# Kernel tuning notes

Measured on AMD Instinct MI355X. Metric: run time of the kernel, lower is better.

Reference implementation:

```python
import jax, jax.numpy as jnp
import numpy as np

R, E, N, B = 64, 100000, 1000000, 4

def setup_inputs() -> dict:
    key = jax.random.key(0)
    k1, k2, k3 = jax.random.split(key, 3)
    p = jax.random.normal(k1, (R,), dtype=jnp.float32)
    edges = jax.random.randint(k2, (R, E, 2), 0, N, dtype=jnp.int64)
    x = jax.random.normal(k3, (B, N), dtype=jnp.float32)
    return {"p": p, "edges": edges, "x": x}

def reference(p, edges, x):
    # _A = sum_r p[r] * (A_r + A_r^T), with A_r[u,v] += 1 per edge (duplicates sum,
    # matching scipy csr_matrix construction). y = x @ _A, i.e.
    # y[b, j] = sum over edges (u,v) of relation r: p[r]*x[b,u] into j=v and p[r]*x[b,v] into j=u.
    num_entities = x.shape[1]
    e = edges.shape[1]
    src = edges[..., 0].reshape(-1)            # [R*E]
    dst = edges[..., 1].reshape(-1)            # [R*E]
    w = jnp.repeat(p, e)                       # [R*E] per-edge relation weight
    # include inverse edges
    srcs = jnp.concatenate([src, dst])         # [2RE]
    dsts = jnp.concatenate([dst, src])         # [2RE]
    ww = jnp.concatenate([w, w])               # [2RE]
    vals = x[:, srcs].T * ww[:, None]          # [2RE, B] gathered & weighted messages
    y = jax.ops.segment_sum(vals, dsts, num_segments=num_entities).T  # [B, N]
    return y
```

## Files before the change

kernel.cpp:

```cpp
#include <hip/hip_runtime.h>
#include <hip/hip_fp16.h>


constexpr int  R_   = 64;
constexpr long E_   = 100000;
constexpr int  N_   = 1000000;
constexpr long RE_  = (long)R_ * E_;
constexpr long M2_  = 2 * RE_;
constexpr int  BSH  = 11;
constexpr int  BUCKET = 1 << BSH;
constexpr int  NB   = (N_ + BUCKET - 1) >> BSH;
constexpr int  NBP  = 512;
constexpr int  EPB  = 4096;
constexpr int  HB   = (int)((RE_ + EPB - 1) / EPB);
constexpr int  RPB  = 2 * EPB;
constexpr int  CH   = 8192;


__global__ __launch_bounds__(256) void k_hist(const int2* __restrict__ edges,
                                              int* __restrict__ g_bcnt) {
    __shared__ int lc[NB];
    for (int i = threadIdx.x; i < NB; i += 256) lc[i] = 0;
    __syncthreads();
    long k0 = (long)blockIdx.x * EPB;
    int lim = (int)min((long)EPB, RE_ - k0);
    for (int i = threadIdx.x; i < lim; i += 256) {
        int2 e = edges[k0 + i];
        atomicAdd(&lc[e.y >> BSH], 1);
        atomicAdd(&lc[e.x >> BSH], 1);
    }
    __syncthreads();
    for (int c = threadIdx.x; c < NB; c += 256)
        g_bcnt[(size_t)c * HB + blockIdx.x] = lc[c];
}

__global__ __launch_bounds__(256) void k_cellscan(const int* __restrict__ g_bcnt,
                                                  int* __restrict__ g_bbase,
                                                  int* __restrict__ ctot) {
    __shared__ int sA[256], sB[256];
    const int c = blockIdx.x, t = threadIdx.x;
    int run = 0;
    for (int chunk = 0; chunk < HB; chunk += 256) {
        int b = chunk + t;
        int v = (b < HB) ? g_bcnt[(size_t)c * HB + b] : 0;
        sA[t] = v;
        __syncthreads();
        int* A = sA; int* B = sB;
        for (int off = 1; off < 256; off <<= 1) {
            int xv = A[t];
            if (t >= off) xv += A[t - off];
            B[t] = xv;
            __syncthreads();
            int* tmp = A; A = B; B = tmp;
        }
        int incl = A[t];
        if (b < HB) g_bbase[(size_t)c * HB + b] = run + incl - v;
        run += A[255];
        __syncthreads();
    }
    if (t == 0) ctot[c] = run;
}

__global__ __launch_bounds__(512) void k_scan(const int* __restrict__ ctot,
                                              int* __restrict__ cbase) {
    __shared__ int sA[NBP], sB[NBP];
    int t = threadIdx.x;
    sA[t] = (t < NB) ? ctot[t] : 0;
    __syncthreads();
    int* A = sA; int* B = sB;
    for (int off = 1; off < NBP; off <<= 1) {
        int xv = A[t];
        if (t >= off) xv += A[t - off];
        B[t] = xv;
        __syncthreads();
        int* tmp = A; A = B; B = tmp;
    }
    if (t < NB) cbase[t] = t ? A[t - 1] : 0;
    if (t == 0) cbase[NB] = A[NB - 1];
}


__global__ __launch_bounds__(1024) void k_srcbin(const int2* __restrict__ edges,
                                                 const int* __restrict__ g_bcnt,
                                                 const int* __restrict__ g_bbase,
                                                 const int* __restrict__ cbase,
                                                 unsigned short* __restrict__ g_sl,
                                                 unsigned* __restrict__ g_dr) {
    __shared__ unsigned l_src[RPB];
    __shared__ unsigned l_dr[RPB];
    __shared__ int sA[NBP], sB[NBP];
    __shared__ int excl[NB], cur[NB], gbase[NB];
    const int t = threadIdx.x, blk = blockIdx.x;
    if (t < NBP) {
        int v = 0;
        if (t < NB) {
            v = g_bcnt[(size_t)t * HB + blk];
            gbase[t] = cbase[t] + g_bbase[(size_t)t * HB + blk];
        }
        sA[t] = v;
    }
    __syncthreads();
    int* A = sA; int* B = sB;
    for (int off = 1; off < NBP; off <<= 1) {
        if (t < NBP) { int v = A[t]; if (t >= off) v += A[t - off]; B[t] = v; }
        __syncthreads();
        int* tmp = A; A = B; B = tmp;
    }
    if (t < NB) { int e = t ? A[t - 1] : 0; excl[t] = e; cur[t] = e; }
    __syncthreads();

    long k0 = (long)blk * EPB;
    int lim = (int)min((long)EPB, RE_ - k0);
    for (int i = t; i < lim; i += 1024) {
        int2 e = edges[k0 + i];
        unsigned r = (unsigned)(k0 + i) / (unsigned)E_;
        int c1 = e.x >> BSH;
        int s1 = atomicAdd(&cur[c1], 1);
        l_src[s1] = (unsigned)e.x;
        l_dr[s1]  = (unsigned)e.y | (r << 20);
        int c2 = e.y >> BSH;
        int s2 = atomicAdd(&cur[c2], 1);
        l_src[s2] = (unsigned)e.y;
        l_dr[s2]  = (unsigned)e.x | (r << 20);
    }
    __syncthreads();
    int total = 2 * lim;
    for (int s = t; s < total; s += 1024) {
        unsigned src = l_src[s];
        int c = (int)(src >> BSH);
        int pos = gbase[c] + (s - excl[c]);
        g_sl[pos] = (unsigned short)(src & (BUCKET - 1));
        __builtin_nontemporal_store(l_dr[s], g_dr + pos);
    }
}


__global__ __launch_bounds__(256) void k_pairhist(const unsigned* __restrict__ g_dr,
                                                  const int* __restrict__ cbase,
                                                  int* __restrict__ pairT) {
    __shared__ int lc[NB];
    const int s = blockIdx.x, t = threadIdx.x;
    for (int i = t; i < NB; i += 256) lc[i] = 0;
    __syncthreads();
    const int lo = cbase[s], hi = cbase[s + 1];
    for (int i = lo + t; i < hi; i += 256) {
        int d = (int)((g_dr[i] & 0xFFFFFu) >> BSH);
        atomicAdd(&lc[d], 1);
    }
    __syncthreads();
    for (int d = t; d < NB; d += 256) pairT[(size_t)d * NB + s] = lc[d];
}

__global__ __launch_bounds__(512) void k_pairscan(const int* __restrict__ cbase,
                                                  int* __restrict__ pairT) {
    __shared__ int sA[NBP], sB[NBP];
    const int d = blockIdx.x, t = threadIdx.x;
    sA[t] = (t < NB) ? pairT[(size_t)d * NB + t] : 0;
    __syncthreads();
    int* A = sA; int* B = sB;
    for (int off = 1; off < NBP; off <<= 1) {
        int v = A[t]; if (t >= off) v += A[t - off]; B[t] = v;
        __syncthreads();
        int* tmp = A; A = B; B = tmp;
    }
    if (t < NB) pairT[(size_t)d * NB + t] = cbase[d] + (t ? A[t - 1] : 0);
}


__global__ __launch_bounds__(1024) void k_msgbuild(const unsigned* __restrict__ g_dr,
                                                   const unsigned short* __restrict__ g_sl,
                                                   const int* __restrict__ cbase,
                                                   const int* __restrict__ pairT,
                                                   const float* __restrict__ p,
                                                   const float* __restrict__ x,
                                                   unsigned short* __restrict__ g_dst2,
                                                   uint2* __restrict__ g_pay2) {
    __shared__ unsigned short l_cell[CH];
    __shared__ unsigned short l_dl[CH];
    __shared__ uint2 l_pay[CH];
    __shared__ uint2 xl[BUCKET];
    __shared__ int sA[NBP], sB[NBP];
    __shared__ int excl[NB], cur[NB], runbase[NB];
    __shared__ float pl[R_];
    const int t = threadIdx.x, s = blockIdx.x;
    if (t < R_) pl[t] = p[t];
    for (int j = t; j < BUCKET; j += 1024) {
        int g = (s << BSH) + j;
        float v0 = 0.f, v1 = 0.f, v2 = 0.f, v3 = 0.f;
        if (g < N_) {
            v0 = x[g]; v1 = x[(long)N_ + g]; v2 = x[2L * N_ + g]; v3 = x[3L * N_ + g];
        }
        __half2 a = __floats2half2_rn(v0, v1);
        __half2 b = __floats2half2_rn(v2, v3);
        xl[j] = make_uint2(__builtin_bit_cast(unsigned, a),
                           __builtin_bit_cast(unsigned, b));
    }
    for (int d = t; d < NB; d += 1024) runbase[d] = pairT[(size_t)d * NB + s];
    __syncthreads();

    const int lo = cbase[s], hi = cbase[s + 1];
    for (int i0 = lo; i0 < hi; i0 += CH) {
        const int cn = min(CH, hi - i0);
        for (int i = t; i < NBP; i += 1024) sA[i] = 0;
        __syncthreads();
        unsigned short mc[8], mdl[8];
        uint2 mp[8];
        #pragma unroll
        for (int j = 0; j < 8; ++j) {
            int k = t + j * 1024;
            mc[j] = 0xFFFF;
            if (k < cn) {
                unsigned dr = g_dr[i0 + k];
                unsigned short sl = g_sl[i0 + k];
                unsigned dst = dr & 0xFFFFFu;
                int c = (int)(dst >> BSH);
                float w = pl[dr >> 20];
                uint2 xv = xl[sl];
                __half2 h0 = __builtin_bit_cast(__half2, xv.x);
                __half2 h1 = __builtin_bit_cast(__half2, xv.y);
                mp[j] = make_uint2(
                    __builtin_bit_cast(unsigned, __floats2half2_rn(w * __low2float(h0), w * __high2float(h0))),
                    __builtin_bit_cast(unsigned, __floats2half2_rn(w * __low2float(h1), w * __high2float(h1))));
                mdl[j] = (unsigned short)(dst & (BUCKET - 1));
                mc[j]  = (unsigned short)c;
                atomicAdd(&sA[c], 1);
            }
        }
        __syncthreads();
        {
            int* A = sA; int* B = sB;
            for (int off = 1; off < NBP; off <<= 1) {
                if (t < NBP) { int v = A[t]; if (t >= off) v += A[t - off]; B[t] = v; }
                __syncthreads();
                int* tmp = A; A = B; B = tmp;
            }
            if (t < NB) { int e = t ? A[t - 1] : 0; excl[t] = e; cur[t] = e; }
        }
        __syncthreads();
        #pragma unroll
        for (int j = 0; j < 8; ++j) {
            if (mc[j] != 0xFFFF) {
                int pos = atomicAdd(&cur[mc[j]], 1);
                l_cell[pos] = mc[j];
                l_dl[pos]   = mdl[j];
                l_pay[pos]  = mp[j];
            }
        }
        __syncthreads();
        for (int s2 = t; s2 < cn; s2 += 1024) {
            int c = l_cell[s2];
            int gpos = runbase[c] + (s2 - excl[c]);
            g_dst2[gpos] = l_dl[s2];
            unsigned long long pk = ((unsigned long long)l_pay[s2].y << 32) | l_pay[s2].x;
            __builtin_nontemporal_store(pk, (unsigned long long*)g_pay2 + gpos);
        }
        __syncthreads();
        for (int d = t; d < NB; d += 1024) runbase[d] += cur[d] - excl[d];
        __syncthreads();
    }
}


__global__ __launch_bounds__(1024) void k_accum(const unsigned short* __restrict__ g_dst,
                                                const uint2* __restrict__ g_pay,
                                                const int* __restrict__ cbase,
                                                float* __restrict__ y) {
    __shared__ unsigned long long accA[BUCKET];
    __shared__ unsigned long long accB[BUCKET];
    const int t = threadIdx.x, b = blockIdx.x;
    for (int i = t; i < BUCKET; i += 1024) { accA[i] = 0ull; accB[i] = 0ull; }
    __syncthreads();
    const int lo = cbase[b], hi = cbase[b + 1];
    for (int i = lo + t; i < hi; i += 1024) {
        int dl = (int)g_dst[i];
        uint2 pay = g_pay[i];
        __half2 h01 = __builtin_bit_cast(__half2, pay.x);
        __half2 h23 = __builtin_bit_cast(__half2, pay.y);
        float f0 = fminf(fmaxf(__low2float(h01),  -31.f), 31.f);
        float f1 = fminf(fmaxf(__high2float(h01), -31.f), 31.f);
        float f2 = fminf(fmaxf(__low2float(h23),  -31.f), 31.f);
        float f3 = fminf(fmaxf(__high2float(h23), -31.f), 31.f);
        unsigned e0 = (unsigned)(__float2int_rn(f0 * 65536.f) + (1 << 21));
        unsigned e1 = (unsigned)(__float2int_rn(f1 * 65536.f) + (1 << 21));
        unsigned e2 = (unsigned)(__float2int_rn(f2 * 65536.f) + (1 << 21));
        unsigned e3 = (unsigned)(__float2int_rn(f3 * 65536.f) + (1 << 21));
        unsigned long long va = (unsigned long long)e0
                              | ((unsigned long long)e1 << 28)
                              | (1ull << 56);
        unsigned long long vb = (unsigned long long)e2
                              | ((unsigned long long)e3 << 28);
        atomicAdd(&accA[dl], va);
        atomicAdd(&accB[dl], vb);
    }
    __syncthreads();
    const int base_e = b << BSH;
    for (int j = t; j < BUCKET; j += 1024) {
        int i = base_e + j;
        if (i < N_) {
            unsigned long long a = accA[j], bb = accB[j];
            long deg  = (long)(a >> 56);
            long bias = deg << 21;
            long c0 = (long)(a & 0xFFFFFFFull) - bias;
            long c1 = (long)((a >> 28) & 0xFFFFFFFull) - bias;
            long c2 = (long)(bb & 0xFFFFFFFull) - bias;
            long c3 = (long)((bb >> 28) & 0xFFFFFFFull) - bias;
            const float sc = 1.f / 65536.f;
            y[i]            = (float)c0 * sc;
            y[(long)N_ + i] = (float)c1 * sc;
            y[2L * N_ + i]  = (float)c2 * sc;
            y[3L * N_ + i]  = (float)c3 * sc;
        }
    }
}


__global__ __launch_bounds__(256) void k_transpose_h(const float* __restrict__ x,
                                                     uint2* __restrict__ xTh) {
    int i = blockIdx.x * 256 + threadIdx.x;
    if (i < N_) {
        __half2 a = __floats2half2_rn(x[i],           x[(long)N_ + i]);
        __half2 b = __floats2half2_rn(x[2L * N_ + i], x[3L * N_ + i]);
        xTh[i] = make_uint2(__builtin_bit_cast(unsigned, a),
                            __builtin_bit_cast(unsigned, b));
    }
}

__global__ __launch_bounds__(1024) void k_bin_g(const int2* __restrict__ edges,
                                                const float* __restrict__ p,
                                                const uint2* __restrict__ xTh,
                                                const int* __restrict__ g_bcnt,
                                                const int* __restrict__ g_bbase,
                                                const int* __restrict__ cbase,
                                                unsigned short* __restrict__ g_dst,
                                                uint2* __restrict__ g_pay) {
    __shared__ int   ldst[RPB];
    __shared__ uint2 lpay[RPB];
    __shared__ int sA[NBP], sB[NBP];
    __shared__ int excl[NB], cur[NB], gbase[NB];
    __shared__ float pl[R_];
    const int t = threadIdx.x, blk = blockIdx.x;
    if (t < NBP) {
        int v = 0;
        if (t < NB) {
            v = g_bcnt[(size_t)t * HB + blk];
            gbase[t] = cbase[t] + g_bbase[(size_t)t * HB + blk];
        }
        sA[t] = v;
    }
    if (t < R_) pl[t] = p[t];
    __syncthreads();
    int* A = sA; int* B = sB;
    for (int off = 1; off < NBP; off <<= 1) {
        if (t < NBP) { int xv = A[t]; if (t >= off) xv += A[t - off]; B[t] = xv; }
        __syncthreads();
        int* tmp = A; A = B; B = tmp;
    }
    if (t < NB) { int e = t ? A[t - 1] : 0; excl[t] = e; cur[t] = e; }
    __syncthreads();
    long k0 = (long)blk * EPB;
    int lim = (int)min((long)EPB, RE_ - k0);
    for (int i = t; i < lim; i += 1024) {
        int2 e = edges[k0 + i];
        float w = pl[(unsigned)(k0 + i) / (unsigned)E_];
        uint2 xu = xTh[e.x];
        uint2 xv = xTh[e.y];
        __half2 a0 = __builtin_bit_cast(__half2, xu.x);
        __half2 a1 = __builtin_bit_cast(__half2, xu.y);
        uint2 pv = make_uint2(
            __builtin_bit_cast(unsigned, __floats2half2_rn(w * __low2float(a0), w * __high2float(a0))),
            __builtin_bit_cast(unsigned, __floats2half2_rn(w * __low2float(a1), w * __high2float(a1))));
        __half2 b0 = __builtin_bit_cast(__half2, xv.x);
        __half2 b1 = __builtin_bit_cast(__half2, xv.y);
        uint2 pu = make_uint2(
            __builtin_bit_cast(unsigned, __floats2half2_rn(w * __low2float(b0), w * __high2float(b0))),
            __builtin_bit_cast(unsigned, __floats2half2_rn(w * __low2float(b1), w * __high2float(b1))));
        int cy = e.y >> BSH;
        int s1 = atomicAdd(&cur[cy], 1);
        ldst[s1] = e.y;
        lpay[s1] = pv;
        int cx = e.x >> BSH;
        int s2 = atomicAdd(&cur[cx], 1);
        ldst[s2] = e.x;
        lpay[s2] = pu;
    }
    __syncthreads();
    int total = 2 * lim;
    for (int s = t; s < total; s += 1024) {
        int dst = ldst[s];
        int c = dst >> BSH;
        int pos = gbase[c] + (s - excl[c]);
        g_dst[pos] = (unsigned short)(dst & (BUCKET - 1));
        g_pay[pos] = lpay[s];
    }
}


__global__ __launch_bounds__(256) void k_scatter_direct(const int2* __restrict__ edges,
                                                        const float* __restrict__ p,
                                                        const float* __restrict__ x,
                                                        float* __restrict__ y) {
    const long stride = (long)gridDim.x * blockDim.x;
    for (long k = (long)blockIdx.x * blockDim.x + threadIdx.x; k < RE_; k += stride) {
        int2 e = edges[k];
        float w = p[(int)(k / E_)];
        #pragma unroll
        for (int b = 0; b < 4; ++b) {
            float xu = x[(long)b * N_ + e.x];
            float xv = x[(long)b * N_ + e.y];
            atomicAdd(&y[(long)b * N_ + e.y], w * xu);
            atomicAdd(&y[(long)b * N_ + e.x], w * xv);
        }
    }
}

extern "C" void kernel_launch(void* const* d_in, const int* in_sizes, int n_in,
                              void* d_out, int out_size, void* d_ws, size_t ws_size,
                              hipStream_t stream) {
    const float* p     = (const float*)d_in[0];
    const int*   edges = (const int*)d_in[1];
    const float* x     = (const float*)d_in[2];
    float*       y     = (float*)d_out;

    const size_t pay_bytes   = (size_t)M2_ * 8;
    const size_t dr_bytes    = (size_t)M2_ * 4;
    const size_t sl_bytes    = (size_t)M2_ * 2;
    const size_t dst2_bytes  = (size_t)M2_ * 2;
    const size_t bcnt_bytes  = (size_t)NB * HB * 4;
    const size_t pair_bytes  = (size_t)NB * NB * 4;
    const size_t ctot_bytes  = (size_t)NB * 4;
    const size_t cbase_bytes = (size_t)(NB + 1) * 4;
    const size_t xTh_bytes   = (size_t)N_ * 8;

    const size_t need_new = pay_bytes + dr_bytes + sl_bytes + dst2_bytes
                          + 2 * bcnt_bytes + pair_bytes + ctot_bytes + cbase_bytes;
    const size_t need_r8  = xTh_bytes + pay_bytes + dst2_bytes
                          + 2 * bcnt_bytes + ctot_bytes + cbase_bytes;

    if (ws_size >= need_new) {
        char* ws = (char*)d_ws;
        uint2* g_pay2 = (uint2*)ws;                  ws += pay_bytes;
        unsigned* g_dr = (unsigned*)ws;              ws += dr_bytes;
        int* g_bcnt  = (int*)ws;                     ws += bcnt_bytes;
        int* g_bbase = (int*)ws;                     ws += bcnt_bytes;
        int* pairT   = (int*)ws;                     ws += pair_bytes;
        int* ctot    = (int*)ws;                     ws += ctot_bytes;
        int* cbase   = (int*)ws;                     ws += cbase_bytes;
        unsigned short* g_sl   = (unsigned short*)ws; ws += sl_bytes;
        unsigned short* g_dst2 = (unsigned short*)ws;

        k_hist<<<HB, 256, 0, stream>>>((const int2*)edges, g_bcnt);
        k_cellscan<<<NB, 256, 0, stream>>>(g_bcnt, g_bbase, ctot);
        k_scan<<<1, 512, 0, stream>>>(ctot, cbase);
        k_srcbin<<<HB, 1024, 0, stream>>>((const int2*)edges, g_bcnt, g_bbase,
                                          cbase, g_sl, g_dr);
        k_pairhist<<<NB, 256, 0, stream>>>((const unsigned*)g_dr, cbase, pairT);
        k_pairscan<<<NB, 512, 0, stream>>>(cbase, pairT);
        k_msgbuild<<<NB, 1024, 0, stream>>>((const unsigned*)g_dr,
                                            (const unsigned short*)g_sl,
                                            cbase, pairT, p, x, g_dst2, g_pay2);
        k_accum<<<NB, 1024, 0, stream>>>((const unsigned short*)g_dst2,
                                         (const uint2*)g_pay2, cbase, y);
    } else if (ws_size >= need_r8) {
        char* ws = (char*)d_ws;
        uint2* xTh   = (uint2*)ws;                   ws += xTh_bytes;
        uint2* g_pay = (uint2*)ws;                   ws += pay_bytes;
        int* g_bcnt  = (int*)ws;                     ws += bcnt_bytes;
        int* g_bbase = (int*)ws;                     ws += bcnt_bytes;
        int* ctot    = (int*)ws;                     ws += ctot_bytes;
        int* cbase   = (int*)ws;                     ws += cbase_bytes;
        unsigned short* g_dst = (unsigned short*)ws;

        k_transpose_h<<<(N_ + 255) / 256, 256, 0, stream>>>(x, xTh);
        k_hist<<<HB, 256, 0, stream>>>((const int2*)edges, g_bcnt);
        k_cellscan<<<NB, 256, 0, stream>>>(g_bcnt, g_bbase, ctot);
        k_scan<<<1, 512, 0, stream>>>(ctot, cbase);
        k_bin_g<<<HB, 1024, 0, stream>>>((const int2*)edges, p, (const uint2*)xTh,
                                         g_bcnt, g_bbase, cbase, g_dst, g_pay);
        k_accum<<<NB, 1024, 0, stream>>>((const unsigned short*)g_dst,
                                         (const uint2*)g_pay, cbase, y);
    } else {
        hipMemsetAsync(y, 0, (size_t)out_size * sizeof(float), stream);
        k_scatter_direct<<<8192, 256, 0, stream>>>((const int2*)edges, p, x, y);
    }
}
```

Baseline: 273.1 us.

## Stage only 16-bit indices in LDS for binning and re-read global data on scatter

In k_srcbin and k_msgbuild the per-entry LDS staging of full records (src, dst|rel, cell, dst-local, half payload) is replaced by a 16-bit index permutation. During the scatter pass the edge or dr/sl data is re-read from global memory and the payload is computed at that point. The smaller LDS footprint permits doubling the msgbuild chunk size CH to 16384. The unused xTh fallback path is removed. This trades LDS capacity and bandwidth for extra, partly uncoalesced, global re-reads that are likely to hit in cache.

```diff
diff --git a/kernel.cpp b/kernel.cpp
--- a/kernel.cpp
+++ b/kernel.cpp
@@ -14,7 +14,7 @@
 constexpr int  EPB  = 4096;
 constexpr int  HB   = (int)((RE_ + EPB - 1) / EPB);
 constexpr int  RPB  = 2 * EPB;
-constexpr int  CH   = 8192;
+constexpr int  CH   = 16384;
 
 
 __global__ __launch_bounds__(256) void k_hist(const int2* __restrict__ edges,
@@ -86,8 +86,7 @@
                                                  const int* __restrict__ cbase,
                                                  unsigned short* __restrict__ g_sl,
                                                  unsigned* __restrict__ g_dr) {
-    __shared__ unsigned l_src[RPB];
-    __shared__ unsigned l_dr[RPB];
+    __shared__ unsigned short l_idx[RPB];
     __shared__ int sA[NBP], sB[NBP];
     __shared__ int excl[NB], cur[NB], gbase[NB];
     const int t = threadIdx.x, blk = blockIdx.x;
@@ -109,28 +108,33 @@
     if (t < NB) { int e = t ? A[t - 1] : 0; excl[t] = e; cur[t] = e; }
     __syncthreads();
 
-    long k0 = (long)blk * EPB;
-    int lim = (int)min((long)EPB, RE_ - k0);
-    for (int i = t; i < lim; i += 1024) {
+    const long k0 = (long)blk * EPB;
+    const int lim = (int)min((long)EPB, RE_ - k0);
+    #pragma unroll
+    for (int j = 0; j < EPB / 1024; ++j) {
+        int i = t + j * 1024;
+        if (i < lim) {
+            int2 e = edges[k0 + i];
+            int p1 = atomicAdd(&cur[e.x >> BSH], 1);
+            l_idx[p1] = (unsigned short)(2 * i);
+            int p2 = atomicAdd(&cur[e.y >> BSH], 1);
+            l_idx[p2] = (unsigned short)(2 * i + 1);
+        }
+    }
+    __syncthreads();
+    const int total = 2 * lim;
+    #pragma unroll 4
+    for (int s = t; s < total; s += 1024) {
+        int idx = l_idx[s];
+        int i = idx >> 1;
         int2 e = edges[k0 + i];
         unsigned r = (unsigned)(k0 + i) / (unsigned)E_;
-        int c1 = e.x >> BSH;
-        int s1 = atomicAdd(&cur[c1], 1);
-        l_src[s1] = (unsigned)e.x;
-        l_dr[s1]  = (unsigned)e.y | (r << 20);
-        int c2 = e.y >> BSH;
-        int s2 = atomicAdd(&cur[c2], 1);
-        l_src[s2] = (unsigned)e.y;
-        l_dr[s2]  = (unsigned)e.x | (r << 20);
-    }
-    __syncthreads();
-    int total = 2 * lim;
-    for (int s = t; s < total; s += 1024) {
-        unsigned src = l_src[s];
-        int c = (int)(src >> BSH);
+        int src, dst;
+        if (idx & 1) { src = e.y; dst = e.x; } else { src = e.x; dst = e.y; }
+        int c = src >> BSH;
         int pos = gbase[c] + (s - excl[c]);
         g_sl[pos] = (unsigned short)(src & (BUCKET - 1));
-        __builtin_nontemporal_store(l_dr[s], g_dr + pos);
+        __builtin_nontemporal_store((unsigned)dst | (r << 20), g_dr + pos);
     }
 }
 
@@ -174,10 +178,8 @@
                                                    const float* __restrict__ p,
                                                    const float* __restrict__ x,
                                                    unsigned short* __restrict__ g_dst2,
-                                                   uint2* __restrict__ g_pay2) {
-    __shared__ unsigned short l_cell[CH];
-    __shared__ unsigned short l_dl[CH];
-    __shared__ uint2 l_pay[CH];
+                                                   unsigned long long* __restrict__ g_pay2) {
+    __shared__ unsigned short l_idx[CH];
     __shared__ uint2 xl[BUCKET];
     __shared__ int sA[NBP], sB[NBP];
     __shared__ int excl[NB], cur[NB], runbase[NB];
@@ -201,28 +203,16 @@
     const int lo = cbase[s], hi = cbase[s + 1];
     for (int i0 = lo; i0 < hi; i0 += CH) {
         const int cn = min(CH, hi - i0);
-        for (int i = t; i < NBP; i += 1024) sA[i] = 0;
-        __syncthreads();
-        unsigned short mc[8], mdl[8];
-        uint2 mp[8];
+        if (t < NBP) sA[t] = 0;
+        __syncthreads();
+        unsigned short mc[CH / 1024];
         #pragma unroll
-        for (int j = 0; j < 8; ++j) {
+        for (int j = 0; j < CH / 1024; ++j) {
             int k = t + j * 1024;
             mc[j] = 0xFFFF;
             if (k < cn) {
-                unsigned dr = g_dr[i0 + k];
-                unsigned short sl = g_sl[i0 + k];
-                unsigned dst = dr & 0xFFFFFu;
-                int c = (int)(dst >> BSH);
-                float w = pl[dr >> 20];
-                uint2 xv = xl[sl];
-                __half2 h0 = __builtin_bit_cast(__half2, xv.x);
-                __half2 h1 = __builtin_bit_cast(__half2, xv.y);
-                mp[j] = make_uint2(
-                    __builtin_bit_cast(unsigned, __floats2half2_rn(w * __low2float(h0), w * __high2float(h0))),
-                    __builtin_bit_cast(unsigned, __floats2half2_rn(w * __low2float(h1), w * __high2float(h1))));
-                mdl[j] = (unsigned short)(dst & (BUCKET - 1));
-                mc[j]  = (unsigned short)c;
+                int c = (int)((g_dr[i0 + k] & 0xFFFFFu) >> BSH);
+                mc[j] = (unsigned short)c;
                 atomicAdd(&sA[c], 1);
             }
         }
@@ -238,21 +228,32 @@
         }
         __syncthreads();
         #pragma unroll
-        for (int j = 0; j < 8; ++j) {
+        for (int j = 0; j < CH / 1024; ++j) {
             if (mc[j] != 0xFFFF) {
                 int pos = atomicAdd(&cur[mc[j]], 1);
-                l_cell[pos] = mc[j];
-                l_dl[pos]   = mdl[j];
-                l_pay[pos]  = mp[j];
+                l_idx[pos] = (unsigned short)(t + j * 1024);
             }
         }
         __syncthreads();
+        #pragma unroll 4
         for (int s2 = t; s2 < cn; s2 += 1024) {
-            int c = l_cell[s2];
+            int idx = l_idx[s2];
+            unsigned dr = g_dr[i0 + idx];
+            unsigned short sl = g_sl[i0 + idx];
+            unsigned dst = dr & 0xFFFFFu;
+            int c = (int)(dst >> BSH);
+            float w = pl[dr >> 20];
+            uint2 xv = xl[sl];
+            __half2 h0 = __builtin_bit_cast(__half2, xv.x);
+            __half2 h1 = __builtin_bit_cast(__half2, xv.y);
+            unsigned plo = __builtin_bit_cast(unsigned,
+                __floats2half2_rn(w * __low2float(h0), w * __high2float(h0)));
+            unsigned phi = __builtin_bit_cast(unsigned,
+                __floats2half2_rn(w * __low2float(h1), w * __high2float(h1)));
             int gpos = runbase[c] + (s2 - excl[c]);
-            g_dst2[gpos] = l_dl[s2];
-            unsigned long long pk = ((unsigned long long)l_pay[s2].y << 32) | l_pay[s2].x;
-            __builtin_nontemporal_store(pk, (unsigned long long*)g_pay2 + gpos);
+            g_dst2[gpos] = (unsigned short)(dst & (BUCKET - 1));
+            __builtin_nontemporal_store(((unsigned long long)phi << 32) | plo,
+                                        g_pay2 + gpos);
         }
         __syncthreads();
         for (int d = t; d < NB; d += 1024) runbase[d] += cur[d] - excl[d];
@@ -314,87 +315,6 @@
 }
 
 
-__global__ __launch_bounds__(256) void k_transpose_h(const float* __restrict__ x,
-                                                     uint2* __restrict__ xTh) {
-    int i = blockIdx.x * 256 + threadIdx.x;
-    if (i < N_) {
-        __half2 a = __floats2half2_rn(x[i],           x[(long)N_ + i]);
-        __half2 b = __floats2half2_rn(x[2L * N_ + i], x[3L * N_ + i]);
-        xTh[i] = make_uint2(__builtin_bit_cast(unsigned, a),
-                            __builtin_bit_cast(unsigned, b));
-    }
-}
-
-__global__ __launch_bounds__(1024) void k_bin_g(const int2* __restrict__ edges,
-                                                const float* __restrict__ p,
-                                                const uint2* __restrict__ xTh,
-                                                const int* __restrict__ g_bcnt,
-                                                const int* __restrict__ g_bbase,
-                                                const int* __restrict__ cbase,
-                                                unsigned short* __restrict__ g_dst,
-                                                uint2* __restrict__ g_pay) {
-    __shared__ int   ldst[RPB];
-    __shared__ uint2 lpay[RPB];
-    __shared__ int sA[NBP], sB[NBP];
-    __shared__ int excl[NB], cur[NB], gbase[NB];
-    __shared__ float pl[R_];
-    const int t = threadIdx.x, blk = blockIdx.x;
-    if (t < NBP) {
-        int v = 0;
-        if (t < NB) {
-            v = g_bcnt[(size_t)t * HB + blk];
-            gbase[t] = cbase[t] + g_bbase[(size_t)t * HB + blk];
-        }
-        sA[t] = v;
-    }
-    if (t < R_) pl[t] = p[t];
-    __syncthreads();
-    int* A = sA; int* B = sB;
-    for (int off = 1; off < NBP; off <<= 1) {
-        if (t < NBP) { int xv = A[t]; if (t >= off) xv += A[t - off]; B[t] = xv; }
-        __syncthreads();
-        int* tmp = A; A = B; B = tmp;
-    }
-    if (t < NB) { int e = t ? A[t - 1] : 0; excl[t] = e; cur[t] = e; }
-    __syncthreads();
-    long k0 = (long)blk * EPB;
-    int lim = (int)min((long)EPB, RE_ - k0);
-    for (int i = t; i < lim; i += 1024) {
-        int2 e = edges[k0 + i];
-        float w = pl[(unsigned)(k0 + i) / (unsigned)E_];
-        uint2 xu = xTh[e.x];
-        uint2 xv = xTh[e.y];
-        __half2 a0 = __builtin_bit_cast(__half2, xu.x);
-        __half2 a1 = __builtin_bit_cast(__half2, xu.y);
-        uint2 pv = make_uint2(
-            __builtin_bit_cast(unsigned, __floats2half2_rn(w * __low2float(a0), w * __high2float(a0))),
-            __builtin_bit_cast(unsigned, __floats2half2_rn(w * __low2float(a1), w * __high2float(a1))));
-        __half2 b0 = __builtin_bit_cast(__half2, xv.x);
-        __half2 b1 = __builtin_bit_cast(__half2, xv.y);
-        uint2 pu = make_uint2(
-            __builtin_bit_cast(unsigned, __floats2half2_rn(w * __low2float(b0), w * __high2float(b0))),
-            __builtin_bit_cast(unsigned, __floats2half2_rn(w * __low2float(b1), w * __high2float(b1))));
-        int cy = e.y >> BSH;
-        int s1 = atomicAdd(&cur[cy], 1);
-        ldst[s1] = e.y;
-        lpay[s1] = pv;
-        int cx = e.x >> BSH;
-        int s2 = atomicAdd(&cur[cx], 1);
-        ldst[s2] = e.x;
-        lpay[s2] = pu;
-    }
-    __syncthreads();
-    int total = 2 * lim;
-    for (int s = t; s < total; s += 1024) {
-        int dst = ldst[s];
-        int c = dst >> BSH;
-        int pos = gbase[c] + (s - excl[c]);
-        g_dst[pos] = (unsigned short)(dst & (BUCKET - 1));
-        g_pay[pos] = lpay[s];
-    }
-}
-
-
 __global__ __launch_bounds__(256) void k_scatter_direct(const int2* __restrict__ edges,
                                                         const float* __restrict__ p,
                                                         const float* __restrict__ x,
@@ -429,16 +349,13 @@
     const size_t pair_bytes  = (size_t)NB * NB * 4;
     const size_t ctot_bytes  = (size_t)NB * 4;
     const size_t cbase_bytes = (size_t)(NB + 1) * 4;
-    const size_t xTh_bytes   = (size_t)N_ * 8;
-
-    const size_t need_new = pay_bytes + dr_bytes + sl_bytes + dst2_bytes
-                          + 2 * bcnt_bytes + pair_bytes + ctot_bytes + cbase_bytes;
-    const size_t need_r8  = xTh_bytes + pay_bytes + dst2_bytes
-                          + 2 * bcnt_bytes + ctot_bytes + cbase_bytes;
-
-    if (ws_size >= need_new) {
+
+    const size_t need = pay_bytes + dr_bytes + sl_bytes + dst2_bytes
+                      + 2 * bcnt_bytes + pair_bytes + ctot_bytes + cbase_bytes;
+
+    if (ws_size >= need) {
         char* ws = (char*)d_ws;
-        uint2* g_pay2 = (uint2*)ws;                  ws += pay_bytes;
+        unsigned long long* g_pay2 = (unsigned long long*)ws;  ws += pay_bytes;
         unsigned* g_dr = (unsigned*)ws;              ws += dr_bytes;
         int* g_bcnt  = (int*)ws;                     ws += bcnt_bytes;
         int* g_bbase = (int*)ws;                     ws += bcnt_bytes;
@@ -460,24 +377,6 @@
                                             cbase, pairT, p, x, g_dst2, g_pay2);
         k_accum<<<NB, 1024, 0, stream>>>((const unsigned short*)g_dst2,
                                          (const uint2*)g_pay2, cbase, y);
-    } else if (ws_size >= need_r8) {
-        char* ws = (char*)d_ws;
-        uint2* xTh   = (uint2*)ws;                   ws += xTh_bytes;
-        uint2* g_pay = (uint2*)ws;                   ws += pay_bytes;
-        int* g_bcnt  = (int*)ws;                     ws += bcnt_bytes;
-        int* g_bbase = (int*)ws;                     ws += bcnt_bytes;
-        int* ctot    = (int*)ws;                     ws += ctot_bytes;
-        int* cbase   = (int*)ws;                     ws += cbase_bytes;
-        unsigned short* g_dst = (unsigned short*)ws;
-
-        k_transpose_h<<<(N_ + 255) / 256, 256, 0, stream>>>(x, xTh);
-        k_hist<<<HB, 256, 0, stream>>>((const int2*)edges, g_bcnt);
-        k_cellscan<<<NB, 256, 0, stream>>>(g_bcnt, g_bbase, ctot);
-        k_scan<<<1, 512, 0, stream>>>(ctot, cbase);
-        k_bin_g<<<HB, 1024, 0, stream>>>((const int2*)edges, p, (const uint2*)xTh,
-                                         g_bcnt, g_bbase, cbase, g_dst, g_pay);
-        k_accum<<<NB, 1024, 0, stream>>>((const unsigned short*)g_dst,
-                                         (const uint2*)g_pay, cbase, y);
     } else {
         hipMemsetAsync(y, 0, (size_t)out_size * sizeof(float), stream);
         k_scatter_direct<<<8192, 256, 0, stream>>>((const int2*)edges, p, x, y);
```

Measured after the change: 306.4 us. 12.2% more time.
